# Kernel optimization log

Measured on AMD Instinct MI355X. Metric: run time of the kernel, lower is better.

Reference implementation:

```python
import jax, jax.numpy as jnp
import numpy as np

NUM_HEADS = 8


def setup_inputs() -> dict:
    key = jax.random.key(0)
    ks = jax.random.split(key, 7)
    b, t, prompt_dim, emb_dim = 2, 4096, 256, 512
    hidden = emb_dim  # head_dim=None -> hidden_dim = emb_dim
    def xavier(k, fan_in, fan_out):
        limit = np.sqrt(6.0 / (fan_in + fan_out)).astype(np.float32)
        return jax.random.uniform(k, (fan_in, fan_out), jnp.float32, -limit, limit)
    return {
        "prompt": jax.random.normal(ks[0], (b, t, prompt_dim), jnp.float32),
        "Wp": xavier(ks[1], prompt_dim, emb_dim),
        "bp": jnp.zeros((emb_dim,), jnp.float32),
        "Wqkv": xavier(ks[2], emb_dim, 3 * hidden),
        "bqkv": jnp.zeros((3 * hidden,), jnp.float32),
        "Wo": xavier(ks[3], hidden, prompt_dim),
        "bo": jnp.zeros((prompt_dim,), jnp.float32),
    }


def reference(prompt, Wp, bp, Wqkv, bqkv, Wo, bo):
    # prompt_proj
    x = prompt @ Wp + bp                      # [b, t, emb_dim]
    b, t, c = x.shape
    qkv = x @ Wqkv + bqkv                     # [b, t, 3*hidden]
    q, k, v = jnp.split(qkv, 3, axis=2)
    def to_heads(z):
        return z.reshape(b, t, NUM_HEADS, -1).transpose(0, 2, 1, 3)  # [b, h, t, d]
    q, k, v = to_heads(q), to_heads(k), to_heads(v)
    d = k.shape[-1]
    scores = jnp.einsum("bhid,bhjd->bhij", q, k) / jnp.sqrt(jnp.float32(d))
    attn = jax.nn.softmax(scores, axis=-1)    # dropout = identity (eval)
    out = jnp.einsum("bhij,bhjd->bhid", attn, v)
    out = out.transpose(0, 2, 1, 3).reshape(b, t, -1)  # [b, t, hidden]
    return out @ Wo + bo                      # [b, t, prompt_dim]
```

## Files before the change

### kernel.cpp

```cpp
#include <hip/hip_runtime.h>
#include <math.h>
#include <stdint.h>


typedef unsigned short u16;
typedef __attribute__((ext_vector_type(8))) __bf16 bf16x8;
typedef __attribute__((ext_vector_type(4))) __bf16 bf16x4;
typedef __attribute__((ext_vector_type(4))) float f32x4;

#define AS1 __attribute__((address_space(1)))
#define AS3 __attribute__((address_space(3)))

__device__ __forceinline__ void async16(const void* g, void* l) {
  __builtin_amdgcn_global_load_lds((const AS1 void*)g, (AS3 void*)l, 16, 0, 0);
}

__device__ __forceinline__ u16 f2bf(float f) {
  union { float f; unsigned u; } c; c.f = f;
  return (u16)((c.u + 0x7fffu + ((c.u >> 16) & 1u)) >> 16);
}

__device__ __forceinline__ float bf2f(u16 u) {
  union { unsigned x; float f; } z; z.x = (unsigned)u << 16; return z.f;
}

__global__ void prep_kernel(const float* __restrict__ prompt, u16* __restrict__ pbf,
                            const float* __restrict__ Wp, const float* __restrict__ Wqkv,
                            const float* __restrict__ Wo, u16* __restrict__ woT,
                            const float* __restrict__ bp, const float* __restrict__ bqkv,
                            float* __restrict__ bfused, u16* __restrict__ wfT) {
  __shared__ u16 Asf[64 * 40];
  __shared__ u16 Bsf[64 * 32];
  __shared__ float red[256];
  const int bid = blockIdx.x, tid = threadIdx.x;
  if (bid < 96) {
    const int k0 = (bid & 3) * 64, n0 = (bid >> 2) * 64;
    const int lane = tid & 63, w = tid >> 6;
    const int wr = w >> 1, wc = w & 1;
    const int lr = lane >> 4, lc = lane & 15;
    f32x4 acc[2][2];
#pragma unroll
    for (int a = 0; a < 2; a++)
#pragma unroll
      for (int b = 0; b < 2; b++) acc[a][b] = (f32x4){0.f, 0.f, 0.f, 0.f};
    for (int e0 = 0; e0 < 512; e0 += 32) {
      {
        const int er = tid >> 3, ng = (tid & 7) * 8;
        float4 v1 = *(const float4*)&Wqkv[(e0 + er) * 1536 + n0 + ng];
        float4 v2 = *(const float4*)&Wqkv[(e0 + er) * 1536 + n0 + ng + 4];
        Asf[(ng + 0) * 40 + er] = f2bf(v1.x); Asf[(ng + 1) * 40 + er] = f2bf(v1.y);
        Asf[(ng + 2) * 40 + er] = f2bf(v1.z); Asf[(ng + 3) * 40 + er] = f2bf(v1.w);
        Asf[(ng + 4) * 40 + er] = f2bf(v2.x); Asf[(ng + 5) * 40 + er] = f2bf(v2.y);
        Asf[(ng + 6) * 40 + er] = f2bf(v2.z); Asf[(ng + 7) * 40 + er] = f2bf(v2.w);
      }
      {
        const int kr = tid >> 2, ec = (tid & 3) * 8;
        float4 w1 = *(const float4*)&Wp[(k0 + kr) * 512 + e0 + ec];
        float4 w2 = *(const float4*)&Wp[(k0 + kr) * 512 + e0 + ec + 4];
        u16 tmp[8] = {f2bf(w1.x), f2bf(w1.y), f2bf(w1.z), f2bf(w1.w),
                      f2bf(w2.x), f2bf(w2.y), f2bf(w2.z), f2bf(w2.w)};
        *(uint4*)&Bsf[kr * 32 + ec] = *(const uint4*)&tmp[0];
      }
      __syncthreads();
      bf16x8 af[2], bf2[2];
#pragma unroll
      for (int mi = 0; mi < 2; mi++)
        af[mi] = *(const bf16x8*)&Asf[(wr * 32 + mi * 16 + lc) * 40 + lr * 8];
#pragma unroll
      for (int nj = 0; nj < 2; nj++)
        bf2[nj] = *(const bf16x8*)&Bsf[(wc * 32 + nj * 16 + lc) * 32 + lr * 8];
#pragma unroll
      for (int mi = 0; mi < 2; mi++)
#pragma unroll
        for (int nj = 0; nj < 2; nj++)
          acc[mi][nj] = __builtin_amdgcn_mfma_f32_16x16x32_bf16(af[mi], bf2[nj], acc[mi][nj], 0, 0, 0);
      __syncthreads();
    }
#pragma unroll
    for (int mi = 0; mi < 2; mi++)
#pragma unroll
      for (int nj = 0; nj < 2; nj++)
#pragma unroll
        for (int r = 0; r < 4; r++)
          wfT[(n0 + wr * 32 + mi * 16 + 4 * lr + r) * 256 + k0 + wc * 32 + nj * 16 + lc] =
              f2bf(acc[mi][nj][r]);
  } else if (bid < 120) {
    const int nloc = tid & 63, slice = tid >> 6;
    const int n = (bid - 96) * 64 + nloc;
    float s = 0.f;
#pragma unroll 8
    for (int e = slice * 128; e < slice * 128 + 128; e++) s += bp[e] * Wqkv[e * 1536 + n];
    red[tid] = s;
    __syncthreads();
    if (slice == 0)
      bfused[n] = red[nloc] + red[64 + nloc] + red[128 + nloc] + red[192 + nloc] + bqkv[n];
  } else if (bid < 632) {
    int j = (bid - 120) * 256 + tid;
    int n = j >> 9, k = j & 511;
    woT[j] = f2bf(Wo[k * 256 + n]);
  } else {
    int i = (bid - 632) * 256 + tid;
    float4 v = ((const float4*)prompt)[i];
    ushort4 o;
    o.x = f2bf(v.x); o.y = f2bf(v.y); o.z = f2bf(v.z); o.w = f2bf(v.w);
    ((ushort4*)pbf)[i] = o;
  }
}

__global__ __launch_bounds__(256) void gemm_qkv(
    const u16* __restrict__ A, const u16* __restrict__ Bt, const float* __restrict__ bias,
    u16* __restrict__ qO, u16* __restrict__ kO, u16* __restrict__ vO, int K) {
  constexpr int TM = 128, MI = 4, NJ = 4;
  __shared__ __align__(16) u16 As[2][TM * 32];
  __shared__ __align__(16) u16 Bs[2][TM * 32];
  const int tid = threadIdx.x;
  const int lane = tid & 63, w = tid >> 6;
  const int wr = w >> 1, wc = w & 1;
  const int lr = lane >> 4, lc = lane & 15;
  const long tileM = (long)blockIdx.y * 128;
  const long tileN = (long)blockIdx.x * 128;

  f32x4 acc[MI][NJ];
#pragma unroll
  for (int a = 0; a < MI; a++)
#pragma unroll
    for (int b = 0; b < NJ; b++) acc[a][b] = (f32x4){0.f, 0.f, 0.f, 0.f};

  const int r0 = lane >> 2;
  const int blk = lane & 3;

  auto stage = [&](int buf, int k0) {
#pragma unroll
    for (int i = 0; i < 2; i++) {
      int r = w * 32 + i * 16 + r0;
      int g = (blk ^ ((r >> 1) & 3)) << 3;
      async16(A + (tileM + r) * (long)K + k0 + g, (void*)&As[buf][(w * 32 + i * 16) * 32]);
      async16(Bt + (tileN + r) * (long)K + k0 + g, (void*)&Bs[buf][(w * 32 + i * 16) * 32]);
    }
  };

  stage(0, 0);
  for (int k0 = 0; k0 < K; k0 += 32) {
    const int cur = (k0 >> 5) & 1;
    stage(cur ^ 1, (k0 + 32 < K) ? k0 + 32 : 0);
    asm volatile("s_waitcnt vmcnt(4)" ::: "memory");
    asm volatile("s_barrier" ::: "memory");

    bf16x8 af[MI], bfv[NJ];
#pragma unroll
    for (int mi = 0; mi < MI; mi++) {
      int r = wr * 64 + mi * 16 + lc;
      af[mi] = *(const bf16x8*)&As[cur][r * 32 + ((lr ^ ((r >> 1) & 3)) << 3)];
    }
#pragma unroll
    for (int nj = 0; nj < NJ; nj++) {
      int r = wc * 64 + nj * 16 + lc;
      bfv[nj] = *(const bf16x8*)&Bs[cur][r * 32 + ((lr ^ ((r >> 1) & 3)) << 3)];
    }
#pragma unroll
    for (int mi = 0; mi < MI; mi++)
#pragma unroll
      for (int nj = 0; nj < NJ; nj++)
        acc[mi][nj] = __builtin_amdgcn_mfma_f32_16x16x32_bf16(af[mi], bfv[nj], acc[mi][nj], 0, 0, 0);
    asm volatile("s_barrier" ::: "memory");
  }

#pragma unroll
  for (int mi = 0; mi < MI; mi++)
#pragma unroll
    for (int nj = 0; nj < NJ; nj++) {
      long col = tileN + wc * 64 + nj * 16 + lc;
      float bcol = bias[col];
      long row0 = tileM + wr * 64 + mi * 16 + lr * 4;
      int sec = (int)(col >> 9);
      int c2 = (int)(col & 511);
      int h = c2 >> 6, d = c2 & 63;
      long pl = (row0 >> 12) * 8 + h;
      long t0 = row0 & 4095;
      if (sec == 2) {
        ushort4 pk;
        pk.x = f2bf(acc[mi][nj][0] + bcol);
        pk.y = f2bf(acc[mi][nj][1] + bcol);
        pk.z = f2bf(acc[mi][nj][2] + bcol);
        pk.w = f2bf(acc[mi][nj][3] + bcol);
        *(ushort4*)&vO[(pl * 64 + d) * 4096 + t0] = pk;
      } else {
        u16* dst = sec ? kO : qO;
        const float sc = sec ? 1.f : 0.18033688f;
#pragma unroll
        for (int r = 0; r < 4; r++)
          dst[((pl * 4096 + t0 + r) << 6) + d] = f2bf((acc[mi][nj][r] + bcol) * sc);
      }
    }
}

__global__ __launch_bounds__(256) void flash_attn(
    const u16* __restrict__ Q, const u16* __restrict__ Kg,
    const u16* __restrict__ VTg, u16* __restrict__ Op, float* __restrict__ lp) {
  __shared__ __align__(16) u16 KV[2][8192];
  __shared__ __align__(16) u16 Ps[4 * 2048];

  const int tid = threadIdx.x, lane = tid & 63, w = tid >> 6;
  const int lr = lane >> 4, lc = lane & 15;
  const int plane = blockIdx.y;
  const int split = blockIdx.z;
  const long pbase = (long)plane << 18;
  const int qr0 = blockIdx.x * 128 + w * 32;
  const int tj0 = split * 32;

  bf16x8 bq[2][2];
#pragma unroll
  for (int qi = 0; qi < 2; qi++)
#pragma unroll
    for (int kk = 0; kk < 2; kk++)
      bq[qi][kk] = *(const bf16x8*)&Q[pbase + (long)(qr0 + qi * 16 + lc) * 64 + kk * 32 + lr * 8];

  bf16x8 ones;
#pragma unroll
  for (int u = 0; u < 8; u++) ones[u] = (__bf16)1.0f;

  f32x4 o[2][4], o1[2];
#pragma unroll
  for (int mi = 0; mi < 2; mi++) {
    o1[mi] = (f32x4){0.f, 0.f, 0.f, 0.f};
#pragma unroll
    for (int nj = 0; nj < 4; nj++) o[mi][nj] = (f32x4){0.f, 0.f, 0.f, 0.f};
  }

  const int krow = lane >> 3, kblk = lane & 7;

  auto stage = [&](int buf, int tj) {
    const u16* kS = Kg + pbase + (long)tj * 4096;
    const u16* vS = VTg + pbase + (long)tj * 64;
#pragma unroll
    for (int i = 0; i < 2; i++) {
      int row = w * 16 + i * 8 + krow;
      async16(kS + (long)row * 64 + ((kblk ^ (row & 7)) << 3),
              (void*)&KV[buf][(w * 16 + i * 8) * 64]);
    }
#pragma unroll
    for (int i = 0; i < 2; i++) {
      int d = w * 16 + i * 8 + krow;
      async16(vS + (long)d * 4096 + ((kblk ^ (d & 7)) << 3),
              (void*)&KV[buf][4096 + (w * 16 + i * 8) * 64]);
    }
  };

  stage(0, tj0);
  for (int j = 0; j < 32; j++) {
    const int cur = j & 1;
    stage(cur ^ 1, (j + 1 < 32) ? tj0 + j + 1 : tj0);
    asm volatile("s_waitcnt vmcnt(4)" ::: "memory");
    asm volatile("s_barrier" ::: "memory");

    const u16* Ks = &KV[cur][0];
    const u16* Vt = &KV[cur][4096];

    f32x4 s[4][2];
#pragma unroll
    for (int ki = 0; ki < 4; ki++)
#pragma unroll
      for (int qi = 0; qi < 2; qi++) s[ki][qi] = (f32x4){0.f, 0.f, 0.f, 0.f};
#pragma unroll
    for (int ki = 0; ki < 4; ki++) {
      const int row = ki * 16 + lc;
      bf16x8 ak[2];
#pragma unroll
      for (int kk = 0; kk < 2; kk++)
        ak[kk] = *(const bf16x8*)&Ks[row * 64 + (((kk * 4 + lr) ^ (row & 7)) << 3)];
#pragma unroll
      for (int qi = 0; qi < 2; qi++)
#pragma unroll
        for (int kk = 0; kk < 2; kk++)
          s[ki][qi] = __builtin_amdgcn_mfma_f32_16x16x32_bf16(ak[kk], bq[qi][kk], s[ki][qi], 0, 0, 0);
    }

#pragma unroll
    for (int qi = 0; qi < 2; qi++) {
      const int pb = w * 2048 + (qi * 16 + lc) * 64 + 4 * (lr & 1);
#pragma unroll
      for (int ki = 0; ki < 4; ki++) {
        bf16x4 pk;
        pk[0] = (__bf16)__builtin_amdgcn_exp2f(s[ki][qi][0]);
        pk[1] = (__bf16)__builtin_amdgcn_exp2f(s[ki][qi][1]);
        pk[2] = (__bf16)__builtin_amdgcn_exp2f(s[ki][qi][2]);
        pk[3] = (__bf16)__builtin_amdgcn_exp2f(s[ki][qi][3]);
        *(bf16x4*)&Ps[pb + (((2 * ki + (lr >> 1)) ^ (lc & 7)) << 3)] = pk;
      }
    }

#pragma unroll
    for (int kk = 0; kk < 2; kk++) {
      bf16x8 ap[2];
#pragma unroll
      for (int mi = 0; mi < 2; mi++)
        ap[mi] = *(const bf16x8*)&Ps[w * 2048 + (mi * 16 + lc) * 64 + (((kk * 4 + lr) ^ (lc & 7)) << 3)];
#pragma unroll
      for (int nj = 0; nj < 4; nj++) {
        const int row = nj * 16 + lc;
        bf16x8 bv = *(const bf16x8*)&Vt[row * 64 + (((kk * 4 + lr) ^ (row & 7)) << 3)];
#pragma unroll
        for (int mi = 0; mi < 2; mi++)
          o[mi][nj] = __builtin_amdgcn_mfma_f32_16x16x32_bf16(ap[mi], bv, o[mi][nj], 0, 0, 0);
      }
#pragma unroll
      for (int mi = 0; mi < 2; mi++)
        o1[mi] = __builtin_amdgcn_mfma_f32_16x16x32_bf16(ap[mi], ones, o1[mi], 0, 0, 0);
    }
    asm volatile("s_barrier" ::: "memory");
  }

  const int bb = plane >> 3, h = plane & 7;
  u16* Ob = Op + (long)split * 4194304;
#pragma unroll
  for (int mi = 0; mi < 2; mi++)
#pragma unroll
    for (int r = 0; r < 4; r++) {
      long t = qr0 + mi * 16 + 4 * lr + r;
#pragma unroll
      for (int nj = 0; nj < 4; nj++)
        Ob[(((long)(bb * 4096 + t) * 8 + h) << 6) + nj * 16 + lc] = f2bf(o[mi][nj][r]);
      if (lc == 0) lp[((split * 16 + plane) << 12) + t] = o1[mi][r];
    }
}

__global__ void reduce_kernel(u16* __restrict__ Op, const float* __restrict__ lp) {
  int i = blockIdx.x * 256 + threadIdx.x;
  int row = i >> 7;
  int c4 = (i & 127) << 2;
  int h = c4 >> 6;
  int b = row >> 12, t = row & 4095;
  float l = lp[((b * 8 + h) << 12) + t] + lp[65536 + ((b * 8 + h) << 12) + t];
  float inv = 1.f / l;
  long idx = (long)row * 512 + c4;
  ushort4 a = *(const ushort4*)&Op[idx];
  ushort4 c = *(const ushort4*)&Op[4194304 + idx];
  ushort4 o;
  o.x = f2bf((bf2f(a.x) + bf2f(c.x)) * inv);
  o.y = f2bf((bf2f(a.y) + bf2f(c.y)) * inv);
  o.z = f2bf((bf2f(a.z) + bf2f(c.z)) * inv);
  o.w = f2bf((bf2f(a.w) + bf2f(c.w)) * inv);
  *(ushort4*)&Op[idx] = o;
}

__global__ __launch_bounds__(256) void gemm_out(
    const u16* __restrict__ A, const u16* __restrict__ Bt, const float* __restrict__ bias,
    float* __restrict__ outf) {
  constexpr int K = 512;
  __shared__ __align__(16) u16 As[2][64 * 32];
  __shared__ __align__(16) u16 Bs[2][64 * 32];
  const int tid = threadIdx.x;
  const int lane = tid & 63, w = tid >> 6;
  const int wr = w >> 1, wc = w & 1;
  const int lr = lane >> 4, lc = lane & 15;
  const long tileM = (long)blockIdx.y * 64;
  const long tileN = (long)blockIdx.x * 64;

  f32x4 acc[2][2];
#pragma unroll
  for (int a = 0; a < 2; a++)
#pragma unroll
    for (int b = 0; b < 2; b++) acc[a][b] = (f32x4){0.f, 0.f, 0.f, 0.f};

  const int r0 = lane >> 2;
  const int blk = lane & 3;

  auto stage = [&](int buf, int k0) {
    int r = w * 16 + r0;
    int g = (blk ^ ((r >> 1) & 3)) << 3;
    async16(A + (tileM + r) * (long)K + k0 + g, (void*)&As[buf][(w * 16) * 32]);
    async16(Bt + (tileN + r) * (long)K + k0 + g, (void*)&Bs[buf][(w * 16) * 32]);
  };

  stage(0, 0);
  for (int k0 = 0; k0 < K; k0 += 32) {
    const int cur = (k0 >> 5) & 1;
    stage(cur ^ 1, (k0 + 32 < K) ? k0 + 32 : 0);
    asm volatile("s_waitcnt vmcnt(2)" ::: "memory");
    asm volatile("s_barrier" ::: "memory");

    bf16x8 af[2], bfv[2];
#pragma unroll
    for (int mi = 0; mi < 2; mi++) {
      int r = wr * 32 + mi * 16 + lc;
      af[mi] = *(const bf16x8*)&As[cur][r * 32 + ((lr ^ ((r >> 1) & 3)) << 3)];
    }
#pragma unroll
    for (int nj = 0; nj < 2; nj++) {
      int r = wc * 32 + nj * 16 + lc;
      bfv[nj] = *(const bf16x8*)&Bs[cur][r * 32 + ((lr ^ ((r >> 1) & 3)) << 3)];
    }
#pragma unroll
    for (int mi = 0; mi < 2; mi++)
#pragma unroll
      for (int nj = 0; nj < 2; nj++)
        acc[mi][nj] = __builtin_amdgcn_mfma_f32_16x16x32_bf16(af[mi], bfv[nj], acc[mi][nj], 0, 0, 0);
    asm volatile("s_barrier" ::: "memory");
  }

#pragma unroll
  for (int mi = 0; mi < 2; mi++)
#pragma unroll
    for (int nj = 0; nj < 2; nj++) {
      long col = tileN + wc * 32 + nj * 16 + lc;
      float bcol = bias[col];
      long row0 = tileM + wr * 32 + mi * 16 + lr * 4;
#pragma unroll
      for (int r = 0; r < 4; r++)
        outf[(row0 + r) * 256 + col] = acc[mi][nj][r] + bcol;
    }
}

extern "C" void kernel_launch(void* const* d_in, const int* in_sizes, int n_in,
                              void* d_out, int out_size, void* d_ws, size_t ws_size,
                              hipStream_t stream) {
  const float* prompt = (const float*)d_in[0];
  const float* Wp = (const float*)d_in[1];
  const float* bp = (const float*)d_in[2];
  const float* Wqkv = (const float*)d_in[3];
  const float* bqkv = (const float*)d_in[4];
  const float* Wo = (const float*)d_in[5];
  const float* bo = (const float*)d_in[6];
  float* out = (float*)d_out;

  char* ws = (char*)d_ws;
  const size_t MiB = 1024 * 1024;
  u16* qb     = (u16*)(ws + 0);
  u16* kb     = (u16*)(ws + 8 * MiB);
  u16* vb     = (u16*)(ws + 16 * MiB);
  u16* pbf    = (u16*)(ws + 24 * MiB);
  float* lpp  = (float*)(ws + 24 * MiB);
  u16* Op     = (u16*)(ws + 28 * MiB);
  u16* woT    = (u16*)(ws + 44 * MiB);
  u16* wfT    = (u16*)(ws + 44 * MiB + 256 * 1024);
  float* bfused = (float*)(ws + 45 * MiB);

  prep_kernel<<<dim3(2680), dim3(256), 0, stream>>>(
      prompt, pbf, Wp, Wqkv, Wo, woT, bp, bqkv, bfused, wfT);

  gemm_qkv<<<dim3(12, 64), dim3(256), 0, stream>>>(
      pbf, wfT, bfused, qb, kb, vb, 256);

  flash_attn<<<dim3(32, 16, 2), dim3(256), 0, stream>>>(qb, kb, vb, Op, lpp);

  reduce_kernel<<<dim3(4096), dim3(256), 0, stream>>>(Op, lpp);

  gemm_out<<<dim3(4, 128), dim3(256), 0, stream>>>(Op, woT, bo, out);
}
```

Measured before the change: 207.5 us.

## Fuse split-KV reduction into output GEMM and widen flash attention blocks

Removes the separate reduce kernel by combining the two split-KV partial outputs and normalising by the summed row sums while loading A tiles in gemm_out. Flash attention now uses 512-thread blocks covering 256 query rows, so each K/V tile staged in shared memory serves twice as many waves. This saves a launch and a full read/write pass over the partial outputs. In exchange, the GEMM's A operand now uses synchronous global loads plus conversion inside the main loop rather than async prefetch, and attention block occupancy changes.

```diff
diff --git a/kernel.cpp b/kernel.cpp
--- a/kernel.cpp
+++ b/kernel.cpp
@@ -18,10 +18,6 @@
 __device__ __forceinline__ u16 f2bf(float f) {
   union { float f; unsigned u; } c; c.f = f;
   return (u16)((c.u + 0x7fffu + ((c.u >> 16) & 1u)) >> 16);
-}
-
-__device__ __forceinline__ float bf2f(u16 u) {
-  union { unsigned x; float f; } z; z.x = (unsigned)u << 16; return z.f;
 }
 
 __global__ void prep_kernel(const float* __restrict__ prompt, u16* __restrict__ pbf,
@@ -194,18 +190,18 @@
     }
 }
 
-__global__ __launch_bounds__(256) void flash_attn(
+__global__ __launch_bounds__(512) void flash_attn(
     const u16* __restrict__ Q, const u16* __restrict__ Kg,
     const u16* __restrict__ VTg, u16* __restrict__ Op, float* __restrict__ lp) {
   __shared__ __align__(16) u16 KV[2][8192];
-  __shared__ __align__(16) u16 Ps[4 * 2048];
+  __shared__ __align__(16) u16 Ps[8 * 2048];
 
   const int tid = threadIdx.x, lane = tid & 63, w = tid >> 6;
   const int lr = lane >> 4, lc = lane & 15;
   const int plane = blockIdx.y;
   const int split = blockIdx.z;
   const long pbase = (long)plane << 18;
-  const int qr0 = blockIdx.x * 128 + w * 32;
+  const int qr0 = blockIdx.x * 256 + w * 32;
   const int tj0 = split * 32;
 
   bf16x8 bq[2][2];
@@ -232,25 +228,18 @@
   auto stage = [&](int buf, int tj) {
     const u16* kS = Kg + pbase + (long)tj * 4096;
     const u16* vS = VTg + pbase + (long)tj * 64;
-#pragma unroll
-    for (int i = 0; i < 2; i++) {
-      int row = w * 16 + i * 8 + krow;
-      async16(kS + (long)row * 64 + ((kblk ^ (row & 7)) << 3),
-              (void*)&KV[buf][(w * 16 + i * 8) * 64]);
-    }
-#pragma unroll
-    for (int i = 0; i < 2; i++) {
-      int d = w * 16 + i * 8 + krow;
-      async16(vS + (long)d * 4096 + ((kblk ^ (d & 7)) << 3),
-              (void*)&KV[buf][4096 + (w * 16 + i * 8) * 64]);
-    }
+    int row = w * 8 + krow;
+    async16(kS + (long)row * 64 + ((kblk ^ (row & 7)) << 3),
+            (void*)&KV[buf][(w * 8) * 64]);
+    async16(vS + (long)row * 4096 + ((kblk ^ (row & 7)) << 3),
+            (void*)&KV[buf][4096 + (w * 8) * 64]);
   };
 
   stage(0, tj0);
   for (int j = 0; j < 32; j++) {
     const int cur = j & 1;
     stage(cur ^ 1, (j + 1 < 32) ? tj0 + j + 1 : tj0);
-    asm volatile("s_waitcnt vmcnt(4)" ::: "memory");
+    asm volatile("s_waitcnt vmcnt(2)" ::: "memory");
     asm volatile("s_barrier" ::: "memory");
 
     const u16* Ks = &KV[cur][0];
@@ -324,27 +313,9 @@
     }
 }
 
-__global__ void reduce_kernel(u16* __restrict__ Op, const float* __restrict__ lp) {
-  int i = blockIdx.x * 256 + threadIdx.x;
-  int row = i >> 7;
-  int c4 = (i & 127) << 2;
-  int h = c4 >> 6;
-  int b = row >> 12, t = row & 4095;
-  float l = lp[((b * 8 + h) << 12) + t] + lp[65536 + ((b * 8 + h) << 12) + t];
-  float inv = 1.f / l;
-  long idx = (long)row * 512 + c4;
-  ushort4 a = *(const ushort4*)&Op[idx];
-  ushort4 c = *(const ushort4*)&Op[4194304 + idx];
-  ushort4 o;
-  o.x = f2bf((bf2f(a.x) + bf2f(c.x)) * inv);
-  o.y = f2bf((bf2f(a.y) + bf2f(c.y)) * inv);
-  o.z = f2bf((bf2f(a.z) + bf2f(c.z)) * inv);
-  o.w = f2bf((bf2f(a.w) + bf2f(c.w)) * inv);
-  *(ushort4*)&Op[idx] = o;
-}
-
 __global__ __launch_bounds__(256) void gemm_out(
-    const u16* __restrict__ A, const u16* __restrict__ Bt, const float* __restrict__ bias,
+    const u16* __restrict__ Op, const float* __restrict__ lp,
+    const u16* __restrict__ Bt, const float* __restrict__ bias,
     float* __restrict__ outf) {
   constexpr int K = 512;
   __shared__ __align__(16) u16 As[2][64 * 32];
@@ -365,18 +336,39 @@
   const int r0 = lane >> 2;
   const int blk = lane & 3;
 
-  auto stage = [&](int buf, int k0) {
+  auto stageB = [&](int buf, int k0) {
     int r = w * 16 + r0;
     int g = (blk ^ ((r >> 1) & 3)) << 3;
-    async16(A + (tileM + r) * (long)K + k0 + g, (void*)&As[buf][(w * 16) * 32]);
     async16(Bt + (tileN + r) * (long)K + k0 + g, (void*)&Bs[buf][(w * 16) * 32]);
   };
 
-  stage(0, 0);
+  const int ar = tid >> 2, ablk = tid & 3;
+  const long arow = tileM + ar;
+  const int ab = (int)(arow >> 12), at = (int)(arow & 4095);
+
+  auto stageA = [&](int buf, int k0) {
+    int h = k0 >> 6;
+    float l0 = lp[(long)((ab * 8 + h) << 12) + at];
+    float l1 = lp[(long)((16 * 4096 * 4) + 0) + 0];
+    (void)l1;
+    float l = l0 + lp[(long)(((16 + ab * 8 + h)) << 12) + at];
+    float inv = 1.f / l;
+    long idx = arow * 512 + k0 + ablk * 8;
+    bf16x8 v0 = *(const bf16x8*)&Op[idx];
+    bf16x8 v1 = *(const bf16x8*)&Op[4194304 + idx];
+    u16 tmp[8];
+#pragma unroll
+    for (int e = 0; e < 8; e++)
+      tmp[e] = f2bf(((float)v0[e] + (float)v1[e]) * inv);
+    *(uint4*)&As[buf][ar * 32 + ((ablk ^ ((ar >> 1) & 3)) << 3)] = *(const uint4*)&tmp[0];
+  };
+
+  stageB(0, 0);
   for (int k0 = 0; k0 < K; k0 += 32) {
     const int cur = (k0 >> 5) & 1;
-    stage(cur ^ 1, (k0 + 32 < K) ? k0 + 32 : 0);
-    asm volatile("s_waitcnt vmcnt(2)" ::: "memory");
+    stageB(cur ^ 1, (k0 + 32 < K) ? k0 + 32 : 0);
+    stageA(cur, k0);
+    asm volatile("s_waitcnt vmcnt(1) lgkmcnt(0)" ::: "memory");
     asm volatile("s_barrier" ::: "memory");
 
     bf16x8 af[2], bfv[2];
@@ -441,9 +433,7 @@
   gemm_qkv<<<dim3(12, 64), dim3(256), 0, stream>>>(
       pbf, wfT, bfused, qb, kb, vb, 256);
 
-  flash_attn<<<dim3(32, 16, 2), dim3(256), 0, stream>>>(qb, kb, vb, Op, lpp);
-
-  reduce_kernel<<<dim3(4096), dim3(256), 0, stream>>>(Op, lpp);
-
-  gemm_out<<<dim3(4, 128), dim3(256), 0, stream>>>(Op, woT, bo, out);
-}
+  flash_attn<<<dim3(16, 16, 2), dim3(512), 0, stream>>>(qb, kb, vb, Op, lpp);
+
+  gemm_out<<<dim3(4, 128), dim3(256), 0, stream>>>(Op, lpp, woT, bo, out);
+}
```

After: 188.9 us. 1.1x faster.
